# Kernel optimization log

Hardware: AMD Instinct MI355X
Metric: run time of the kernel (lower is better)

The kernel has to match this reference:

```python
import jax, jax.numpy as jnp
import numpy as np

LR, HR, H, D1 = 512, 2048, 4, 200
N = 2 * HR            # 4096 nodes (fully connected graph)
C1 = D1 // H          # 50  per-head dim, layer 1
C2 = HR // H          # 512 per-head dim, layer 2
EPS = 1e-5


def setup_inputs() -> dict:
    key = jax.random.key(0)
    ks = jax.random.split(key, 24)
    lin = lambda k, fi, fo: jax.random.normal(k, (fi, fo), jnp.float32) * 0.02
    vec = lambda k, d: jax.random.normal(k, (d,), jnp.float32) * 0.02
    inp = {"lr_x": jax.random.normal(ks[0], (LR, N), jnp.float32)}
    # TransformerConv 1: lr -> 200 (query/key/value/skip linears, each with bias)
    inp["Wq1"], inp["bq1"] = lin(ks[1], LR, D1), vec(ks[2], D1)
    inp["Wk1"], inp["bk1"] = lin(ks[3], LR, D1), vec(ks[4], D1)
    inp["Wv1"], inp["bv1"] = lin(ks[5], LR, D1), vec(ks[6], D1)
    inp["Ws1"], inp["bs1"] = lin(ks[7], LR, D1), vec(ks[8], D1)
    # GraphNorm 1
    inp["gn1_w"] = 1.0 + 0.1 * jax.random.normal(ks[9], (D1,), jnp.float32)
    inp["gn1_b"] = vec(ks[10], D1)
    inp["gn1_ms"] = 1.0 + 0.1 * jax.random.normal(ks[11], (D1,), jnp.float32)
    # TransformerConv 2: 200 -> 2048
    inp["Wq2"], inp["bq2"] = lin(ks[12], D1, HR), vec(ks[13], HR)
    inp["Wk2"], inp["bk2"] = lin(ks[14], D1, HR), vec(ks[15], HR)
    inp["Wv2"], inp["bv2"] = lin(ks[16], D1, HR), vec(ks[17], HR)
    inp["Ws2"], inp["bs2"] = lin(ks[18], D1, HR), vec(ks[19], HR)
    # GraphNorm 2
    inp["gn2_w"] = 1.0 + 0.1 * jax.random.normal(ks[20], (HR,), jnp.float32)
    inp["gn2_b"] = vec(ks[21], HR)
    inp["gn2_ms"] = 1.0 + 0.1 * jax.random.normal(ks[22], (HR,), jnp.float32)
    return inp


def _transformer_conv(x, Wq, bq, Wk, bk, Wv, bv, Ws, bs, heads, ch):
    # PyG TransformerConv on a fully-connected edge_index == dense multi-head attention
    n = x.shape[0]
    q = (x @ Wq + bq).reshape(n, heads, ch)
    k = (x @ Wk + bk).reshape(n, heads, ch)
    v = (x @ Wv + bv).reshape(n, heads, ch)
    scores = jnp.einsum('ihc,jhc->hij', q, k) / (ch ** 0.5)  # [H, N, N]
    attn = jax.nn.softmax(scores, axis=-1)                   # softmax over source nodes j
    out = jnp.einsum('hij,jhc->ihc', attn, v).reshape(n, heads * ch)
    return out + x @ Ws + bs                                 # root/skip connection


def _graph_norm(x, w, b, ms):
    # PyG GraphNorm: y = w * (x - ms*mean) / sqrt(E[(x - ms*mean)^2] + eps) + b
    mean = jnp.mean(x, axis=0, keepdims=True)
    out = x - mean * ms
    var = jnp.mean(out * out, axis=0, keepdims=True)
    return out * jax.lax.rsqrt(var + EPS) * w + b


def reference(lr_x, Wq1, bq1, Wk1, bk1, Wv1, bv1, Ws1, bs1, gn1_w, gn1_b, gn1_ms,
              Wq2, bq2, Wk2, bk2, Wv2, bv2, Ws2, bs2, gn2_w, gn2_b, gn2_ms):
    h = _transformer_conv(lr_x.T, Wq1, bq1, Wk1, bk1, Wv1, bv1, Ws1, bs1, H, C1)  # [N, 200]
    h = _graph_norm(h, gn1_w, gn1_b, gn1_ms)
    h2 = _transformer_conv(h, Wq2, bq2, Wk2, bk2, Wv2, bv2, Ws2, bs2, H, C2)      # [N, HR]
    h2 = _graph_norm(h2, gn2_w, gn2_b, gn2_ms).T                                  # [HR, N]
    h2 = h2 / jnp.linalg.norm(h2, axis=1, keepdims=True)
    return jax.nn.relu(h2 @ h2.T)                                                 # [HR, HR]
```

## Files before the change

kernel.cpp:

```cpp
#include <hip/hip_runtime.h>
#include <math.h>

typedef unsigned int u32;
typedef unsigned short ushort_t;
typedef __attribute__((ext_vector_type(8))) short short8;
typedef __attribute__((ext_vector_type(4))) float f32x4;

__device__ __forceinline__ ushort_t f2bf(float x) {
  u32 u = __float_as_uint(x);
  u32 r = (u + 0x7fffu + ((u >> 16) & 1u)) >> 16;
  return (ushort_t)r;
}
__device__ __forceinline__ float bf2f(u32 s) {
  return __uint_as_float(s << 16);
}
__device__ __forceinline__ void ld4bf(const ushort_t* p, float* o) {
  uint2 u = *(const uint2*)p;
  o[0] = bf2f(u.x & 0xffffu); o[1] = bf2f(u.x >> 16);
  o[2] = bf2f(u.y & 0xffffu); o[3] = bf2f(u.y >> 16);
}

__device__ __forceinline__ float block_sum256(float v, float* red) {
  #pragma unroll
  for (int o = 32; o > 0; o >>= 1) v += __shfl_down(v, o, 64);
  __syncthreads();
  if ((threadIdx.x & 63) == 0) red[threadIdx.x >> 6] = v;
  __syncthreads();
  return red[0] + red[1] + red[2] + red[3];
}

__global__ __launch_bounds__(512) void fused_attn1(
    const ushort_t* __restrict__ qk, const ushort_t* __restrict__ v,
    float* __restrict__ oP, float* __restrict__ r1p, float scale)
{
  __shared__ ushort_t Kl[2][4096];
  __shared__ ushort_t Vl[2][4096];
  __shared__ ushort_t Pl[128][80];
  const int t = threadIdx.x;
  const int lane = t & 63;
  const int wv = t >> 6;
  const int h = blockIdx.y;
  const int m0 = blockIdx.x * 128;
  const int z = blockIdx.z;
  const int lr = lane & 15;
  const int hk = lane >> 4;

  short8 aq0, aq1;
  {
    const ushort_t* qrow = qk + (size_t)(m0 + wv * 16 + lr) * 512 + h * 64;
    aq0 = *(const short8*)(qrow + hk * 8);
    aq1 = *(const short8*)(qrow + 32 + hk * 8);
  }

  f32x4 oAcc[4];
  #pragma unroll
  for (int i = 0; i < 4; ++i) oAcc[i] = (f32x4){0.f, 0.f, 0.f, 0.f};
  float racc[4] = {0.f, 0.f, 0.f, 0.f};

  const size_t kbase = (size_t)256 + h * 64;
  const int rS = t >> 3;
  const int cS = t & 7;
  const int lcS = cS ^ (rS & 7);

  {
    const int n0 = z * 16 * 64;
    __builtin_amdgcn_global_load_lds(
        (const __attribute__((address_space(1))) u32*)(qk + (size_t)(n0 + rS) * 512 + kbase + lcS * 8),
        (__attribute__((address_space(3))) u32*)(&Kl[0][t * 8]), 16, 0, 0);
    __builtin_amdgcn_global_load_lds(
        (const __attribute__((address_space(1))) u32*)(v + (size_t)(h * 128 + rS) * 4096 + n0 + lcS * 8),
        (__attribute__((address_space(3))) u32*)(&Vl[0][t * 8]), 16, 0, 0);
  }
  __syncthreads();

  int cur = 0;
  for (int it = 0; it < 16; ++it) {
    if (it + 1 < 16) {
      const int n1 = (z * 16 + it + 1) * 64;
      __builtin_amdgcn_global_load_lds(
          (const __attribute__((address_space(1))) u32*)(qk + (size_t)(n1 + rS) * 512 + kbase + lcS * 8),
          (__attribute__((address_space(3))) u32*)(&Kl[cur ^ 1][t * 8]), 16, 0, 0);
      __builtin_amdgcn_global_load_lds(
          (const __attribute__((address_space(1))) u32*)(v + (size_t)(h * 128 + rS) * 4096 + n1 + lcS * 8),
          (__attribute__((address_space(3))) u32*)(&Vl[cur ^ 1][t * 8]), 16, 0, 0);
    }
    f32x4 sA[4];
    #pragma unroll
    for (int nf = 0; nf < 4; ++nf) {
      const int rl = nf * 16 + lr;
      const char* kb = (const char*)&Kl[cur][0] + rl * 128;
      short8 b0 = *(const short8*)(kb + ((hk ^ (rl & 7)) * 16));
      short8 b1 = *(const short8*)(kb + (((4 + hk) ^ (rl & 7)) * 16));
      f32x4 sa = (f32x4){0.f, 0.f, 0.f, 0.f};
      sa = __builtin_amdgcn_mfma_f32_16x16x32_bf16(aq0, b0, sa, 0, 0, 0);
      sa = __builtin_amdgcn_mfma_f32_16x16x32_bf16(aq1, b1, sa, 0, 0, 0);
      sA[nf] = sa;
    }
    #pragma unroll
    for (int nf = 0; nf < 4; ++nf) {
      #pragma unroll
      for (int r = 0; r < 4; ++r) {
        float e = exp2f(sA[nf][r] * scale);
        racc[r] += e;
        Pl[wv * 16 + hk * 4 + r][nf * 16 + lr] = f2bf(e);
      }
    }
    short8 ap0 = *(const short8*)&Pl[wv * 16 + lr][hk * 8];
    short8 ap1 = *(const short8*)&Pl[wv * 16 + lr][32 + hk * 8];
    #pragma unroll
    for (int ff = 0; ff < 4; ++ff) {
      const int rl = ff * 16 + lr;
      const char* vb = (const char*)&Vl[cur][0] + rl * 128;
      short8 b0 = *(const short8*)(vb + ((hk ^ (rl & 7)) * 16));
      short8 b1 = *(const short8*)(vb + (((4 + hk) ^ (rl & 7)) * 16));
      oAcc[ff] = __builtin_amdgcn_mfma_f32_16x16x32_bf16(ap0, b0, oAcc[ff], 0, 0, 0);
      oAcc[ff] = __builtin_amdgcn_mfma_f32_16x16x32_bf16(ap1, b1, oAcc[ff], 0, 0, 0);
    }
    __syncthreads();
    cur ^= 1;
  }

  #pragma unroll
  for (int r = 0; r < 4; ++r) {
    racc[r] += __shfl_xor(racc[r], 1);
    racc[r] += __shfl_xor(racc[r], 2);
    racc[r] += __shfl_xor(racc[r], 4);
    racc[r] += __shfl_xor(racc[r], 8);
  }
  if (lr == 0) {
    float* rp = r1p + ((size_t)z * 4 + h) * 4096;
    #pragma unroll
    for (int r = 0; r < 4; ++r) rp[m0 + wv * 16 + hk * 4 + r] = racc[r];
  }
  float* ob = oP + (size_t)z * 512 * 4096;
  #pragma unroll
  for (int ff = 0; ff < 4; ++ff) {
    const size_t fbase = (size_t)(h * 128 + ff * 16 + lr) * 4096;
    #pragma unroll
    for (int r = 0; r < 4; ++r) {
      const int q = m0 + wv * 16 + hk * 4 + r;
      ob[fbase + q] = oAcc[ff][r];
    }
  }
}

__global__ __launch_bounds__(512, 2) void fused_attn2(
    const ushort_t* __restrict__ Tm, const ushort_t* __restrict__ X,
    const ushort_t* __restrict__ Xt, ushort_t* __restrict__ Up, float scale)
{
  __shared__ ushort_t Xl[16384];
  __shared__ ushort_t Xtl[2][16384];
  __shared__ ushort_t Pl[256][66];
  const int t = threadIdx.x;
  const int lane = t & 63;
  const int wv = t >> 6;
  const int h = blockIdx.y;
  const int m0 = blockIdx.x * 256;
  const int z = blockIdx.z;
  const int lr = lane & 15;
  const int hk = lane >> 4;

  short8 tq[2][8];
  #pragma unroll
  for (int qb = 0; qb < 2; ++qb) {
    const ushort_t* trow = Tm + ((size_t)h * 4096 + m0 + wv * 32 + qb * 16 + lr) * 256;
    #pragma unroll
    for (int s = 0; s < 8; ++s) tq[qb][s] = *(const short8*)(trow + s * 32 + hk * 8);
  }

  f32x4 uAcc[16][2];
  #pragma unroll
  for (int i = 0; i < 16; ++i) {
    uAcc[i][0] = (f32x4){0.f, 0.f, 0.f, 0.f};
    uAcc[i][1] = (f32x4){0.f, 0.f, 0.f, 0.f};
  }

  auto stageX = [&](int n0) {
    #pragma unroll
    for (int i = 0; i < 4; ++i) {
      const int st = t + i * 512;
      const int row = st >> 5, ph = st & 31;
      const int lc = (ph & 24) | ((ph & 7) ^ (row & 7));
      __builtin_amdgcn_global_load_lds(
          (const __attribute__((address_space(1))) u32*)(X + (size_t)(n0 + row) * 256 + lc * 8),
          (__attribute__((address_space(3))) u32*)(&Xl[st * 8]), 16, 0, 0);
    }
  };
  auto stageXt = [&](int buf, int n0) {
    #pragma unroll
    for (int i = 0; i < 4; ++i) {
      const int st = t + i * 512;
      const int row = st >> 3, ph = st & 7;
      const int lc = ph ^ (row & 7);
      __builtin_amdgcn_global_load_lds(
          (const __attribute__((address_space(1))) u32*)(Xt + (size_t)row * 4096 + n0 + lc * 8),
          (__attribute__((address_space(3))) u32*)(&Xtl[buf][st * 8]), 16, 0, 0);
    }
  };

  const int base = z * 16;
  stageX(base * 64);
  stageXt(0, base * 64);
  __syncthreads();

  int cur = 0;
  for (int it = 0; it < 16; ++it) {
    if (it + 1 < 16) stageXt(cur ^ 1, (base + it + 1) * 64);
    const char* xb = (const char*)&Xl[0];
    #pragma unroll
    for (int nf = 0; nf < 4; ++nf) {
      const int row = nf * 16 + lr;
      const char* rb = xb + row * 512;
      f32x4 sa0 = (f32x4){0.f, 0.f, 0.f, 0.f};
      f32x4 sa1 = (f32x4){0.f, 0.f, 0.f, 0.f};
      #pragma unroll
      for (int s = 0; s < 8; ++s) {
        const int c = s * 4 + hk;
        const int ph = (c & 24) | ((c & 7) ^ (row & 7));
        short8 xf = *(const short8*)(rb + ph * 16);
        sa0 = __builtin_amdgcn_mfma_f32_16x16x32_bf16(xf, tq[0][s], sa0, 0, 0, 0);
        sa1 = __builtin_amdgcn_mfma_f32_16x16x32_bf16(xf, tq[1][s], sa1, 0, 0, 0);
      }
      #pragma unroll
      for (int r = 0; r < 4; ++r) {
        Pl[wv * 32 + lr][nf * 16 + hk * 4 + r]      = f2bf(exp2f(sa0[r] * scale));
        Pl[wv * 32 + 16 + lr][nf * 16 + hk * 4 + r] = f2bf(exp2f(sa1[r] * scale));
      }
    }
    __syncthreads();
    if (it + 1 < 16) stageX((base + it + 1) * 64);
    short8 p00 = *(const short8*)((const char*)&Pl[wv * 32 + lr][0] + hk * 16);
    short8 p01 = *(const short8*)((const char*)&Pl[wv * 32 + lr][0] + (4 + hk) * 16);
    short8 p10 = *(const short8*)((const char*)&Pl[wv * 32 + 16 + lr][0] + hk * 16);
    short8 p11 = *(const short8*)((const char*)&Pl[wv * 32 + 16 + lr][0] + (4 + hk) * 16);
    const char* xtb = (const char*)&Xtl[cur][0];
    #pragma unroll
    for (int ff = 0; ff < 16; ++ff) {
      const int row = ff * 16 + lr;
      const char* rb2 = xtb + row * 128;
      short8 x0 = *(const short8*)(rb2 + ((hk ^ (row & 7)) * 16));
      short8 x1 = *(const short8*)(rb2 + (((4 + hk) ^ (row & 7)) * 16));
      uAcc[ff][0] = __builtin_amdgcn_mfma_f32_16x16x32_bf16(x0, p00, uAcc[ff][0], 0, 0, 0);
      uAcc[ff][0] = __builtin_amdgcn_mfma_f32_16x16x32_bf16(x1, p01, uAcc[ff][0], 0, 0, 0);
      uAcc[ff][1] = __builtin_amdgcn_mfma_f32_16x16x32_bf16(x0, p10, uAcc[ff][1], 0, 0, 0);
      uAcc[ff][1] = __builtin_amdgcn_mfma_f32_16x16x32_bf16(x1, p11, uAcc[ff][1], 0, 0, 0);
    }
    __syncthreads();
    cur ^= 1;
  }

  ushort_t* ub = Up + (size_t)(z * 4 + h) * 256 * 4096;
  #pragma unroll
  for (int ff = 0; ff < 16; ++ff) {
    #pragma unroll
    for (int qb = 0; qb < 2; ++qb) {
      #pragma unroll
      for (int r = 0; r < 4; ++r) {
        const int a = ff * 16 + hk * 4 + r;
        ub[(size_t)a * 4096 + m0 + wv * 32 + qb * 16 + lr] = f2bf(uAcc[ff][qb][r]);
      }
    }
  }
}

__global__ __launch_bounds__(256) void combine_u(
    const ushort_t* __restrict__ Up, ushort_t* __restrict__ Usum,
    float* __restrict__ r2)
{
  __shared__ float tl[64][65];
  const int t = threadIdx.x;
  const int qt = blockIdx.x;
  const int at = blockIdx.y;
  const int h  = blockIdx.z;
  const int c = t & 63;
  const int rb = t >> 6;
  const size_t PLN = (size_t)4 * 256 * 4096;
  #pragma unroll
  for (int i = 0; i < 16; ++i) {
    const int r = rb + i * 4;
    const int a = at * 64 + r;
    const int q = qt * 64 + c;
    const size_t i0 = ((size_t)h * 256 + a) * 4096 + q;
    float val = bf2f(Up[i0]) + bf2f(Up[PLN + i0])
              + bf2f(Up[2 * PLN + i0]) + bf2f(Up[3 * PLN + i0]);
    tl[r][c] = val;
    if (a == 200) r2[(size_t)h * 4096 + q] = val;
  }
  __syncthreads();
  #pragma unroll
  for (int i = 0; i < 16; ++i) {
    const int r = rb + i * 4;
    const int q = qt * 64 + r;
    const int a = at * 64 + c;
    Usum[((size_t)h * 4096 + q) * 256 + a] = f2bf(tl[c][r]);
  }
}

#define RD_A(bb, mm, cc) (*(const short8*)(lsAc + (bb)*32768 + arow + (mm)*2048 + (cc)))
#define RD_B(bb, nn, cc) (*(const short8*)(lsBc + (bb)*32768 + brow + (nn)*2048 + (cc)))

#define MM8(nn, bv) { \
  acc[0][nn] = __builtin_amdgcn_mfma_f32_16x16x32_bf16(a0, bv, acc[0][nn], 0,0,0); \
  acc[1][nn] = __builtin_amdgcn_mfma_f32_16x16x32_bf16(a1, bv, acc[1][nn], 0,0,0); \
  acc[2][nn] = __builtin_amdgcn_mfma_f32_16x16x32_bf16(a2, bv, acc[2][nn], 0,0,0); \
  acc[3][nn] = __builtin_amdgcn_mfma_f32_16x16x32_bf16(a3, bv, acc[3][nn], 0,0,0); \
  acc[4][nn] = __builtin_amdgcn_mfma_f32_16x16x32_bf16(a4, bv, acc[4][nn], 0,0,0); \
  acc[5][nn] = __builtin_amdgcn_mfma_f32_16x16x32_bf16(a5, bv, acc[5][nn], 0,0,0); \
  acc[6][nn] = __builtin_amdgcn_mfma_f32_16x16x32_bf16(a6, bv, acc[6][nn], 0,0,0); \
  acc[7][nn] = __builtin_amdgcn_mfma_f32_16x16x32_bf16(a7, bv, acc[7][nn], 0,0,0); }

#define STG(BASE, LD, LS, bb, hf, tt) { \
  _Pragma("unroll") \
  for (int ii = 0; ii < 2; ++ii) { \
    const int s_ = t + ii * 512; \
    const int r_ = s_ >> 3; \
    const int lc_ = (s_ & 7) ^ (r_ & 7); \
    __builtin_amdgcn_global_load_lds( \
      (const __attribute__((address_space(1))) u32*)((BASE) + (size_t)((hf) * 128 + r_) * (LD) + (size_t)(tt) * 64 + lc_ * 8), \
      (__attribute__((address_space(3))) u32*)(&(LS)[bb][(hf) * 8192 + s_ * 8]), 16, 0, 0); \
  } }

#define BAR() __builtin_amdgcn_s_barrier()
#define PRIO(x) __builtin_amdgcn_s_setprio(x)

#define GRP(bf, tS1, tS2) { \
  a0=RD_A(bf,0,c0); a1=RD_A(bf,1,c0); a2=RD_A(bf,2,c0); a3=RD_A(bf,3,c0); \
  a4=RD_A(bf,4,c0); a5=RD_A(bf,5,c0); a6=RD_A(bf,6,c0); a7=RD_A(bf,7,c0); \
  b0=RD_B(bf,0,c0); b1=RD_B(bf,1,c0); \
  STG(Ab, lda, lsA, 1-(bf), 1, tS1); STG(Bb, ldb, lsB, 1-(bf), 0, tS1); \
  BAR(); PRIO(1); MM8(0, b0); MM8(1, b1); PRIO(0); BAR(); \
  b2=RD_B(bf,2,c0); b3=RD_B(bf,3,c0); \
  STG(Bb, ldb, lsB, 1-(bf), 1, tS1); \
  BAR(); PRIO(1); MM8(2, b2); MM8(3, b3); PRIO(0); BAR(); \
  a0=RD_A(bf,0,c1); a1=RD_A(bf,1,c1); a2=RD_A(bf,2,c1); a3=RD_A(bf,3,c1); \
  a4=RD_A(bf,4,c1); a5=RD_A(bf,5,c1); a6=RD_A(bf,6,c1); a7=RD_A(bf,7,c1); \
  b0=RD_B(bf,0,c1); b1=RD_B(bf,1,c1); \
  BAR(); PRIO(1); MM8(0, b0); MM8(1, b1); PRIO(0); BAR(); \
  b2=RD_B(bf,2,c1); b3=RD_B(bf,3,c1); \
  STG(Ab, lda, lsA, (bf), 0, tS2); \
  BAR(); PRIO(1); MM8(2, b2); MM8(3, b3); PRIO(0); \
  asm volatile("s_waitcnt vmcnt(2)" ::: "memory"); \
  BAR(); }

template<int CMODE, bool RELU>
__global__ __launch_bounds__(512, 2) void mfma256_8ph(
    const ushort_t* __restrict__ A, const ushort_t* __restrict__ B,
    void* __restrict__ Cv, int lda, int ldb, int ldc,
    int K, int zsplit, size_t zA, size_t zB, size_t zC,
    int bShift, size_t bHead, int Mvalid, float scale)
{
  __shared__ ushort_t lsA[2][16384];
  __shared__ ushort_t lsB[2][16384];
  const int t = threadIdx.x;
  const int gx = gridDim.x;
  const int nwg = gx * gridDim.y;
  const int bid = blockIdx.y * gx + blockIdx.x;
  const int qq = nwg >> 3, rr_ = nwg & 7;
  const int xcd = bid & 7, idx = bid >> 3;
  const int swz = (xcd < rr_ ? xcd * (qq + 1) : rr_ * (qq + 1) + (xcd - rr_) * qq) + idx;
  const int m0 = (swz / gx) * 256;
  const int n0 = (swz % gx) * 256;
  const int z = blockIdx.z;
  int Kc = K, kOff = 0;
  size_t aZ = 0, bZ = 0, cZ = 0;
  if (zsplit > 1) { Kc = K / zsplit; kOff = z * Kc; cZ = (size_t)z * zC; }
  else { aZ = (size_t)z * zA; bZ = (size_t)z * zB; cZ = (size_t)z * zC; }
  const ushort_t* Ab = A + aZ + (size_t)m0 * lda + kOff;
  const ushort_t* Bb = B + bZ + (size_t)n0 * ldb + kOff
                     + (bShift >= 0 ? (size_t)(m0 >> bShift) * bHead : 0);
  const int NT = Kc / 64;

  f32x4 acc[8][4];
  #pragma unroll
  for (int i = 0; i < 8; ++i)
    #pragma unroll
    for (int j = 0; j < 4; ++j) acc[i][j] = (f32x4){0.f, 0.f, 0.f, 0.f};

  const int lane = t & 63;
  const int wv = t >> 6;
  const int wr = (wv >> 2) * 128;
  const int wc = (wv & 3) * 64;
  const int lr = lane & 15;
  const int kc = lane >> 4;
  const int sw = lane & 7;
  const int c0 = (kc ^ sw) * 16;
  const int c1 = c0 ^ 64;
  const int arow = (wr + lr) * 128;
  const int brow = (wc + lr) * 128;
  const char* lsAc = (const char*)lsA;
  const char* lsBc = (const char*)lsB;

  short8 a0, a1, a2, a3, a4, a5, a6, a7, b0, b1, b2, b3;

  STG(Ab, lda, lsA, 0, 0, 0); STG(Ab, lda, lsA, 0, 1, 0);
  STG(Bb, ldb, lsB, 0, 0, 0); STG(Bb, ldb, lsB, 0, 1, 0);
  STG(Ab, lda, lsA, 1, 0, 1);
  asm volatile("s_waitcnt vmcnt(2)" ::: "memory");
  BAR();

  const int NITER = NT >> 1;
  for (int it = 0; it < NITER; ++it) {
    const int tb = 2 * it;
    const int s1 = tb + 1;
    const int s2 = (tb + 2 < NT) ? tb + 2 : 0;
    const int s3 = (tb + 3 < NT) ? tb + 3 : 0;
    GRP(0, s1, s2)
    GRP(1, s2, s3)
  }

  const int row4 = (lane >> 4) * 4;
  const int coln = lane & 15;
  float* Cf = (float*)Cv + cZ;
  ushort_t* Ch = (ushort_t*)Cv + cZ;
  #pragma unroll
  for (int m = 0; m < 8; ++m) {
    #pragma unroll
    for (int r = 0; r < 4; ++r) {
      const int gm = m0 + wr + m * 16 + row4 + r;
      const bool ok = gm < Mvalid;
      #pragma unroll
      for (int n = 0; n < 4; ++n) {
        const int gn = n0 + wc + n * 16 + coln;
        float v = acc[m][n][r] * scale;
        if (RELU) v = fmaxf(v, 0.f);
        if (ok) {
          if (CMODE == 0)      Cf[(size_t)gm * ldc + gn] = v;
          else if (CMODE == 1) Ch[(size_t)gm * ldc + gn] = f2bf(v);
          else                 atomicAdd(&Cf[(size_t)gm * ldc + gn], v);
        }
      }
    }
  }
}

#undef GRP
#undef STG
#undef MM8
#undef RD_A
#undef RD_B

template<int CMODE, bool RELU>
__global__ __launch_bounds__(256) void mfma_bt(
    const ushort_t* __restrict__ A, const ushort_t* __restrict__ B,
    void* __restrict__ Cv, int lda, int ldb, int ldc,
    int K, int Ksplit, size_t zA, size_t zB, size_t zC,
    int bShift, size_t bHead, int mMask, int Mvalid, float scale)
{
  __shared__ ushort_t lsA[2][128 * 32];
  __shared__ ushort_t lsB[2][128 * 32];
  const int t  = threadIdx.x;
  const int m0 = blockIdx.y * 128;
  const int n0 = blockIdx.x * 128;
  const int z = blockIdx.z;
  int Kc = K, kOff = 0;
  size_t aZ = 0, bZ = 0, cZ = 0;
  if (Ksplit > 1) { Kc = K / Ksplit; kOff = z * Kc; cZ = (size_t)z * zC; }
  else { aZ = (size_t)z * zA; bZ = (size_t)z * zB; cZ = (size_t)z * zC; }
  const int NT = Kc / 32;
  const ushort_t* Ab = A + aZ + (size_t)m0 * lda + kOff;
  const ushort_t* Bb = B + bZ + (size_t)n0 * ldb + kOff
                     + (bShift >= 0 ? (size_t)(m0 >> bShift) * bHead : 0);
  const int cs = t & 3;

  f32x4 acc[4][4];
  #pragma unroll
  for (int i = 0; i < 4; ++i)
    #pragma unroll
    for (int j = 0; j < 4; ++j) acc[i][j] = (f32x4){0.f, 0.f, 0.f, 0.f};

  const int lane = t & 63;
  const int wv = t >> 6;
  const int wr = (wv >> 1) * 64;
  const int wc = (wv & 1) * 64;
  const int lr = lane & 15;
  const int kc = lane >> 4;

  int roffA[4], roffB[4];
  #pragma unroll
  for (int m = 0; m < 4; ++m) {
    int ra = wr + m * 16 + lr;
    roffA[m] = ra * 64 + ((kc ^ (ra & 3)) * 16);
    int rb = wc + m * 16 + lr;
    roffB[m] = rb * 64 + ((kc ^ (rb & 3)) * 16);
  }

  auto stage = [&](int buf, int kt) {
    const ushort_t* As = Ab + kt * 32;
    const ushort_t* Bs = Bb + kt * 32;
    #pragma unroll
    for (int i = 0; i < 2; ++i) {
      int s = t + i * 256;
      int r = s >> 2;
      int c = cs ^ (r & 3);
      __builtin_amdgcn_global_load_lds(
          (const __attribute__((address_space(1))) u32*)(As + (size_t)r * lda + c * 8),
          (__attribute__((address_space(3))) u32*)(&lsA[buf][s * 8]), 16, 0, 0);
    }
    #pragma unroll
    for (int i = 0; i < 2; ++i) {
      int s = t + i * 256;
      int r = s >> 2;
      int c = cs ^ (r & 3);
      __builtin_amdgcn_global_load_lds(
          (const __attribute__((address_space(1))) u32*)(Bs + (size_t)r * ldb + c * 8),
          (__attribute__((address_space(3))) u32*)(&lsB[buf][s * 8]), 16, 0, 0);
    }
  };

  stage(0, 0);
  __syncthreads();
  int cur = 0;
  for (int kt = 0; kt < NT; ++kt) {
    if (kt + 1 < NT) stage(cur ^ 1, kt + 1);
    short8 af[4], bfr[4];
    const char* baseA = (const char*)&lsA[cur][0];
    const char* baseB = (const char*)&lsB[cur][0];
    #pragma unroll
    for (int m = 0; m < 4; ++m) af[m]  = *(const short8*)(baseA + roffA[m]);
    #pragma unroll
    for (int n = 0; n < 4; ++n) bfr[n] = *(const short8*)(baseB + roffB[n]);
    #pragma unroll
    for (int m = 0; m < 4; ++m)
      #pragma unroll
      for (int n = 0; n < 4; ++n)
        acc[m][n] = __builtin_amdgcn_mfma_f32_16x16x32_bf16(af[m], bfr[n], acc[m][n], 0, 0, 0);
    __syncthreads();
    cur ^= 1;
  }

  const int row4 = (lane >> 4) * 4;
  const int coln = lane & 15;
  float* Cf = (float*)Cv + cZ;
  ushort_t* Ch = (ushort_t*)Cv + cZ;
  #pragma unroll
  for (int m = 0; m < 4; ++m) {
    #pragma unroll
    for (int r = 0; r < 4; ++r) {
      const int gm = m0 + wr + m * 16 + row4 + r;
      const bool ok = (mMask >= 0) ? ((gm & mMask) < Mvalid) : (gm < Mvalid);
      #pragma unroll
      for (int n = 0; n < 4; ++n) {
        const int gn = n0 + wc + n * 16 + coln;
        float v = acc[m][n][r] * scale;
        if (RELU) v = fmaxf(v, 0.f);
        if (ok) {
          if (CMODE == 0)      Cf[(size_t)gm * ldc + gn] = v;
          else if (CMODE == 1) Ch[(size_t)gm * ldc + gn] = f2bf(v);
          else                 atomicAdd(&Cf[(size_t)gm * ldc + gn], v);
        }
      }
    }
  }
}

__global__ __launch_bounds__(256) void wt_conv(
    const float* __restrict__ W, const float* __restrict__ bias,
    ushort_t* __restrict__ dst, int Mtot, int ldw, int Kv, int Kp,
    int PADH, int VALH)
{
  const int m = blockIdx.x;
  const int h = m / PADH, c0 = m % PADH;
  const int fout = h * VALH + c0;
  const bool valid = (c0 < VALH) && (fout < Mtot);
  for (int k = threadIdx.x; k < Kp; k += blockDim.x) {
    float v = 0.f;
    if (valid) {
      if (k < Kv) v = W[(size_t)k * ldw + fout];
      else if (k == Kv) v = bias[fout];
    }
    dst[(size_t)m * Kp + k] = f2bf(v);
  }
}

__global__ __launch_bounds__(256) void wt_trans(
    const float* __restrict__ W, const float* __restrict__ bias,
    ushort_t* __restrict__ dst)
{
  const int rid = blockIdx.x;
  const int h = rid >> 8, a = rid & 255;
  for (int f = threadIdx.x; f < 512; f += 256) {
    float v = 0.f;
    if (a < 200)       v = W[(size_t)a * 2048 + h * 512 + f];
    else if (a == 200) v = bias[h * 512 + f];
    dst[(size_t)rid * 512 + f] = f2bf(v);
  }
}

__global__ __launch_bounds__(256) void xt_conv(
    const float* __restrict__ h1nT, ushort_t* __restrict__ Xt)
{
  const int a = blockIdx.x;
  for (int q = threadIdx.x; q < 4096; q += 256) {
    float v = (a < 200) ? h1nT[(size_t)a * 4096 + q] : ((a == 200) ? 1.f : 0.f);
    Xt[(size_t)a * 4096 + q] = f2bf(v);
  }
}

__global__ __launch_bounds__(256) void trans_pad(
    const float* __restrict__ src, ushort_t* __restrict__ dst, int Kv, int Kp)
{
  __shared__ float tl[64][65];
  const int t = threadIdx.x;
  const int f0 = blockIdx.x * 64;
  const int i0 = blockIdx.y * 64;
  const int c = t & 63, rbase = t >> 6;
  #pragma unroll
  for (int it = 0; it < 16; ++it) {
    int r = rbase + it * 4;
    int f = f0 + r;
    tl[r][c] = (f < Kv) ? src[(size_t)f * 4096 + i0 + c] : 0.f;
  }
  __syncthreads();
  #pragma unroll
  for (int it = 0; it < 16; ++it) {
    int r = rbase + it * 4;
    int f = f0 + c;
    if (f < Kp) {
      float v = (f < Kv) ? tl[c][r] : ((f == Kv) ? 1.f : 0.f);
      dst[(size_t)(i0 + r) * Kp + f] = f2bf(v);
    }
  }
}

__global__ __launch_bounds__(256) void graph_norm_attn1(
    const float* __restrict__ skip, const float* __restrict__ oP,
    const float* __restrict__ r1p, float* __restrict__ out,
    const float* __restrict__ w, const float* __restrict__ b,
    const float* __restrict__ ms)
{
  __shared__ float red[4];
  const int t = threadIdx.x;
  const int row = blockIdx.x;
  const int h = row / 50;
  const int pr = h * 128 + row % 50;
  const float* sk = skip + (size_t)pr * 4096;
  const size_t OSTR = (size_t)512 * 4096;
  float v[16];
  float s = 0.f;
  #pragma unroll
  for (int e = 0; e < 4; ++e) {
    const int idx = t * 4 + 1024 * e;
    float4 a = *(const float4*)&sk[idx];
    float4 o0 = *(const float4*)&oP[(size_t)pr * 4096 + idx];
    float4 o1 = *(const float4*)&oP[OSTR + (size_t)pr * 4096 + idx];
    float4 o2 = *(const float4*)&oP[2 * OSTR + (size_t)pr * 4096 + idx];
    float4 o3 = *(const float4*)&oP[3 * OSTR + (size_t)pr * 4096 + idx];
    float4 r0 = *(const float4*)&r1p[(size_t)h * 4096 + idx];
    float4 r1 = *(const float4*)&r1p[(size_t)(4 + h) * 4096 + idx];
    float4 r2 = *(const float4*)&r1p[(size_t)(8 + h) * 4096 + idx];
    float4 r3 = *(const float4*)&r1p[(size_t)(12 + h) * 4096 + idx];
    v[e*4+0] = a.x + (o0.x + o1.x + o2.x + o3.x) / (r0.x + r1.x + r2.x + r3.x);
    v[e*4+1] = a.y + (o0.y + o1.y + o2.y + o3.y) / (r0.y + r1.y + r2.y + r3.y);
    v[e*4+2] = a.z + (o0.z + o1.z + o2.z + o3.z) / (r0.z + r1.z + r2.z + r3.z);
    v[e*4+3] = a.w + (o0.w + o1.w + o2.w + o3.w) / (r0.w + r1.w + r2.w + r3.w);
    s += v[e*4+0] + v[e*4+1] + v[e*4+2] + v[e*4+3];
  }
  const float mean = block_sum256(s, red) * (1.f / 4096.f);
  const float sub = mean * ms[row];
  float s2 = 0.f;
  #pragma unroll
  for (int e = 0; e < 16; ++e) { v[e] -= sub; s2 += v[e] * v[e]; }
  const float var = block_sum256(s2, red) * (1.f / 4096.f);
  const float scl = rsqrtf(var + 1e-5f) * w[row];
  const float bb = b[row];
  float* y = out + (size_t)row * 4096;
  #pragma unroll
  for (int e = 0; e < 4; ++e) {
    float o0[4];
    #pragma unroll
    for (int q = 0; q < 4; ++q) o0[q] = v[e * 4 + q] * scl + bb;
    *(float4*)&y[t * 4 + 1024 * e] = *(float4*)&o0[0];
  }
}

__global__ __launch_bounds__(256) void graph_norm_attn2(
    const ushort_t* __restrict__ skip, const ushort_t* __restrict__ O,
    const float* __restrict__ r2, ushort_t* __restrict__ out,
    const float* __restrict__ w, const float* __restrict__ b,
    const float* __restrict__ ms)
{
  __shared__ float red[4];
  const int t = threadIdx.x;
  const int row = blockIdx.x;
  const ushort_t* sk = skip + (size_t)row * 4096;
  const ushort_t* pa = O + (size_t)row * 4096;
  const float* rr = r2 + (size_t)(row >> 9) * 4096;
  float v[16];
  float s = 0.f;
  #pragma unroll
  for (int e = 0; e < 4; ++e) {
    const int idx = t * 4 + 1024 * e;
    float a[4], oa[4];
    ld4bf(&sk[idx], a); ld4bf(&pa[idx], oa);
    float4 rv = *(const float4*)&rr[idx];
    v[e*4+0] = a[0] + oa[0] / rv.x;
    v[e*4+1] = a[1] + oa[1] / rv.y;
    v[e*4+2] = a[2] + oa[2] / rv.z;
    v[e*4+3] = a[3] + oa[3] / rv.w;
    s += v[e*4+0] + v[e*4+1] + v[e*4+2] + v[e*4+3];
  }
  const float mean = block_sum256(s, red) * (1.f / 4096.f);
  const float sub = mean * ms[row];
  float s2 = 0.f;
  #pragma unroll
  for (int e = 0; e < 16; ++e) { v[e] -= sub; s2 += v[e] * v[e]; }
  const float var = block_sum256(s2, red) * (1.f / 4096.f);
  const float scl = rsqrtf(var + 1e-5f) * w[row];
  const float bb = b[row];
  #pragma unroll
  for (int e = 0; e < 16; ++e) v[e] = v[e] * scl + bb;
  float s3 = 0.f;
  #pragma unroll
  for (int e = 0; e < 16; ++e) s3 += v[e] * v[e];
  const float osc = rsqrtf(block_sum256(s3, red));
  ushort_t* y = out + (size_t)row * 4096;
  #pragma unroll
  for (int e = 0; e < 4; ++e) {
    ushort_t o0[4];
    #pragma unroll
    for (int q = 0; q < 4; ++q) o0[q] = f2bf(v[e * 4 + q] * osc);
    *(ushort2*)&y[t * 4 + 1024 * e] = *(ushort2*)&o0[0];
    *(ushort2*)&y[t * 4 + 1024 * e + 2] = *(ushort2*)&o0[2];
  }
}

__global__ __launch_bounds__(256) void add4_relu_bf16(
    const ushort_t* __restrict__ g, float* __restrict__ out)
{
  const size_t i = (size_t)blockIdx.x * 256 + threadIdx.x;
  const size_t ss = (size_t)2048 * 2048;
  float a[4], b[4], c[4], d[4];
  ld4bf(&g[i * 4], a);
  ld4bf(&g[ss + i * 4], b);
  ld4bf(&g[2 * ss + i * 4], c);
  ld4bf(&g[3 * ss + i * 4], d);
  float4 o;
  o.x = fmaxf(a[0] + b[0] + c[0] + d[0], 0.f);
  o.y = fmaxf(a[1] + b[1] + c[1] + d[1], 0.f);
  o.z = fmaxf(a[2] + b[2] + c[2] + d[2], 0.f);
  o.w = fmaxf(a[3] + b[3] + c[3] + d[3], 0.f);
  ((float4*)out)[i] = o;
}

extern "C" void kernel_launch(void* const* d_in, const int* in_sizes, int n_in,
                              void* d_out, int out_size, void* d_ws, size_t ws_size,
                              hipStream_t stream)
{
  (void)in_sizes; (void)n_in; (void)out_size; (void)ws_size;
  const float* lr_x = (const float*)d_in[0];
  const float* Wq1 = (const float*)d_in[1];  const float* bq1 = (const float*)d_in[2];
  const float* Wk1 = (const float*)d_in[3];  const float* bk1 = (const float*)d_in[4];
  const float* Wv1 = (const float*)d_in[5];  const float* bv1 = (const float*)d_in[6];
  const float* Ws1 = (const float*)d_in[7];  const float* bs1 = (const float*)d_in[8];
  const float* gn1w = (const float*)d_in[9]; const float* gn1b = (const float*)d_in[10];
  const float* gn1ms = (const float*)d_in[11];
  const float* Wq2 = (const float*)d_in[12]; const float* bq2 = (const float*)d_in[13];
  const float* Wk2 = (const float*)d_in[14]; const float* bk2 = (const float*)d_in[15];
  const float* Wv2 = (const float*)d_in[16]; const float* bv2 = (const float*)d_in[17];
  const float* Ws2 = (const float*)d_in[18]; const float* bs2 = (const float*)d_in[19];
  const float* gn2w = (const float*)d_in[20]; const float* gn2b = (const float*)d_in[21];
  const float* gn2ms = (const float*)d_in[22];

  char* p = (char*)d_ws;
  auto alloc = [&](size_t bytes) { char* r = p; p += (bytes + 255) & ~(size_t)255; return r; };
  char*     scrA = alloc((size_t)32 * 1024 * 1024);
  ushort_t* xb   = (ushort_t*)alloc((size_t)4096 * 544 * 2);
  ushort_t* qk1b = (ushort_t*)alloc((size_t)4096 * 512 * 2);
  ushort_t* v1b  = (ushort_t*)alloc((size_t)512 * 4096 * 2);
  char*     u0   = alloc((size_t)16 * 1024 * 1024);
  float*    s1p  = (float*)u0;
  float*    h1nT = (float*)   alloc((size_t)200 * 4096 * 4);
  ushort_t* h1nb = (ushort_t*)alloc((size_t)4096 * 256 * 2);
  ushort_t* Wqk1 = (ushort_t*)alloc((size_t)512 * 544 * 2);
  ushort_t* Wv1b = (ushort_t*)alloc((size_t)512 * 544 * 2);
  ushort_t* Ws1p = (ushort_t*)alloc((size_t)512 * 544 * 2);
  ushort_t* Wcat = (ushort_t*)alloc((size_t)4096 * 256 * 2);
  ushort_t* Qt   = (ushort_t*)alloc((size_t)4 * 256 * 512 * 2);
  ushort_t* Kt   = (ushort_t*)alloc((size_t)4 * 256 * 512 * 2);
  ushort_t* Mtall= (ushort_t*)alloc((size_t)4 * 256 * 256 * 2);
  ushort_t* Tall = (ushort_t*)alloc((size_t)4 * 4096 * 256 * 2);
  ushort_t* Xtb  = (ushort_t*)alloc((size_t)256 * 4096 * 2);
  ushort_t* vs2b = (ushort_t*)alloc((size_t)4096 * 4096 * 2);
  ushort_t* Usum = (ushort_t*)alloc((size_t)4 * 4096 * 256 * 2);
  ushort_t* Opl  = (ushort_t*)alloc((size_t)2048 * 4096 * 2);
  float*    r1p  = (float*)   alloc((size_t)16 * 4096 * 4);
  float*    r2   = (float*)   alloc((size_t)4 * 4096 * 4);
  float*    oP   = (float*)scrA;
  ushort_t* UpH  = (ushort_t*)scrA;
  ushort_t* g4   = (ushort_t*)scrA;
  ushort_t* h2b  = (ushort_t*)u0;

  const dim3 b256(256, 1, 1);
  const dim3 b512(512, 1, 1);
  const float LOG2E = 1.4426950408889634f;
  const float sc1e = 0.14142135623730951f * LOG2E;
  const float sc2e = 0.04419417382415922f * LOG2E;

  wt_conv<<<dim3(256),  b256, 0, stream>>>(Wq1, bq1, Wqk1,             200, 200, 512, 544, 64, 50);
  wt_conv<<<dim3(256),  b256, 0, stream>>>(Wk1, bk1, Wqk1 + 256 * 544, 200, 200, 512, 544, 64, 50);
  wt_conv<<<dim3(512),  b256, 0, stream>>>(Wv1, bv1, Wv1b,             200, 200, 512, 544, 128, 50);
  wt_conv<<<dim3(512),  b256, 0, stream>>>(Ws1, bs1, Ws1p,             200, 200, 512, 544, 128, 50);
  wt_conv<<<dim3(2048), b256, 0, stream>>>(Wv2, bv2, Wcat,              2048, 2048, 200, 256, 2048, 2048);
  wt_conv<<<dim3(2048), b256, 0, stream>>>(Ws2, bs2, Wcat + 2048 * 256, 2048, 2048, 200, 256, 2048, 2048);
  wt_trans<<<dim3(1024), b256, 0, stream>>>(Wq2, bq2, Qt);
  wt_trans<<<dim3(1024), b256, 0, stream>>>(Wk2, bk2, Kt);
  trans_pad<<<dim3(9, 64), b256, 0, stream>>>(lr_x, xb, 512, 544);

  mfma_bt<1, false><<<dim3(4, 32), b256, 0, stream>>>(
      xb, Wqk1, qk1b, 544, 544, 512, 544, 1, 0, 0, 0, -1, 0, -1, 4096, 1.f);
  mfma_bt<1, false><<<dim3(32, 4), b256, 0, stream>>>(
      Wv1b, xb, v1b, 544, 544, 4096, 544, 1, 0, 0, 0, -1, 0, -1, 512, 1.f);
  mfma_bt<0, false><<<dim3(32, 4), b256, 0, stream>>>(
      Ws1p, xb, s1p, 544, 544, 4096, 544, 1, 0, 0, 0, -1, 0, 127, 50, 1.f);

  fused_attn1<<<dim3(32, 4, 4), b512, 0, stream>>>(qk1b, v1b, oP, r1p, sc1e);
  graph_norm_attn1<<<dim3(200), b256, 0, stream>>>(s1p, oP, r1p, h1nT, gn1w, gn1b, gn1ms);
  trans_pad<<<dim3(4, 64), b256, 0, stream>>>(h1nT, h1nb, 200, 256);
  xt_conv<<<dim3(256), b256, 0, stream>>>(h1nT, Xtb);

  mfma_bt<1, false><<<dim3(32, 32), b256, 0, stream>>>(
      Wcat, h1nb, vs2b, 256, 256, 4096, 256, 1, 0, 0, 0, -1, 0, -1, 4096, 1.f);

  mfma_bt<1, false><<<dim3(2, 2, 4), b256, 0, stream>>>(
      Kt, Qt, Mtall, 512, 512, 256, 512, 1,
      (size_t)256 * 512, (size_t)256 * 512, (size_t)256 * 256, -1, 0, -1, 256, 1.f);
  mfma_bt<1, false><<<dim3(2, 32, 4), b256, 0, stream>>>(
      h1nb, Mtall, Tall, 256, 256, 256, 256, 1,
      0, (size_t)256 * 256, (size_t)4096 * 256, -1, 0, -1, 4096, 1.f);
  fused_attn2<<<dim3(16, 4, 4), b512, 0, stream>>>(Tall, h1nb, Xtb, UpH, sc2e);
  combine_u<<<dim3(64, 4, 4), b256, 0, stream>>>(UpH, Usum, r2);
  mfma_bt<1, false><<<dim3(32, 16), b256, 0, stream>>>(
      Wcat, Usum, Opl, 256, 256, 4096, 256, 1,
      0, 0, 0, 9, (size_t)4096 * 256, -1, 2048, 1.f);
  graph_norm_attn2<<<dim3(2048), b256, 0, stream>>>(
      vs2b + (size_t)2048 * 4096, Opl, r2, h2b, gn2w, gn2b, gn2ms);

  mfma256_8ph<1, false><<<dim3(8, 8, 4), b512, 0, stream>>>(
      h2b, h2b, g4, 4096, 4096, 2048, 4096, 4,
      0, 0, (size_t)2048 * 2048, -1, 0, 2048, 1.f);
  add4_relu_bf16<<<dim3(4096), b256, 0, stream>>>(g4, (float*)d_out);
}
```

Before: 350.5 us.

## Trim padded layer-2 K dimension to 224 and merge V1/skip GEMMs

Layer 2's inner dimension is 200, padded to 256. The fused attention kernel and several GEMMs now loop over only 224 of those columns (7 k-steps and 14 feature tiles instead of 8 and 16), which skips MFMA work and accumulators on zero padding. The layer-1 value and skip projections are merged into one GEMM writing bf16, and graph_norm_attn1 now reads the skip term as bf16 instead of fp32. The risks are that any data living in columns 224–255 (such as the bias column at index 200) must fall inside the kept range, that the Up rows for features 224–255 are no longer written, and that the skip term loses precision.

```diff
diff --git a/kernel.cpp b/kernel.cpp
--- a/kernel.cpp
+++ b/kernel.cpp
@@ -160,17 +160,17 @@
   const int lr = lane & 15;
   const int hk = lane >> 4;
 
-  short8 tq[2][8];
+  short8 tq[2][7];
   #pragma unroll
   for (int qb = 0; qb < 2; ++qb) {
     const ushort_t* trow = Tm + ((size_t)h * 4096 + m0 + wv * 32 + qb * 16 + lr) * 256;
     #pragma unroll
-    for (int s = 0; s < 8; ++s) tq[qb][s] = *(const short8*)(trow + s * 32 + hk * 8);
-  }
-
-  f32x4 uAcc[16][2];
-  #pragma unroll
-  for (int i = 0; i < 16; ++i) {
+    for (int s = 0; s < 7; ++s) tq[qb][s] = *(const short8*)(trow + s * 32 + hk * 8);
+  }
+
+  f32x4 uAcc[14][2];
+  #pragma unroll
+  for (int i = 0; i < 14; ++i) {
     uAcc[i][0] = (f32x4){0.f, 0.f, 0.f, 0.f};
     uAcc[i][1] = (f32x4){0.f, 0.f, 0.f, 0.f};
   }
@@ -214,7 +214,7 @@
       f32x4 sa0 = (f32x4){0.f, 0.f, 0.f, 0.f};
       f32x4 sa1 = (f32x4){0.f, 0.f, 0.f, 0.f};
       #pragma unroll
-      for (int s = 0; s < 8; ++s) {
+      for (int s = 0; s < 7; ++s) {
         const int c = s * 4 + hk;
         const int ph = (c & 24) | ((c & 7) ^ (row & 7));
         short8 xf = *(const short8*)(rb + ph * 16);
@@ -235,7 +235,7 @@
     short8 p11 = *(const short8*)((const char*)&Pl[wv * 32 + 16 + lr][0] + (4 + hk) * 16);
     const char* xtb = (const char*)&Xtl[cur][0];
     #pragma unroll
-    for (int ff = 0; ff < 16; ++ff) {
+    for (int ff = 0; ff < 14; ++ff) {
       const int row = ff * 16 + lr;
       const char* rb2 = xtb + row * 128;
       short8 x0 = *(const short8*)(rb2 + ((hk ^ (row & 7)) * 16));
@@ -251,7 +251,7 @@
 
   ushort_t* ub = Up + (size_t)(z * 4 + h) * 256 * 4096;
   #pragma unroll
-  for (int ff = 0; ff < 16; ++ff) {
+  for (int ff = 0; ff < 14; ++ff) {
     #pragma unroll
     for (int qb = 0; qb < 2; ++qb) {
       #pragma unroll
@@ -623,7 +623,7 @@
 }
 
 __global__ __launch_bounds__(256) void graph_norm_attn1(
-    const float* __restrict__ skip, const float* __restrict__ oP,
+    const ushort_t* __restrict__ skip, const float* __restrict__ oP,
     const float* __restrict__ r1p, float* __restrict__ out,
     const float* __restrict__ w, const float* __restrict__ b,
     const float* __restrict__ ms)
@@ -633,14 +633,15 @@
   const int row = blockIdx.x;
   const int h = row / 50;
   const int pr = h * 128 + row % 50;
-  const float* sk = skip + (size_t)pr * 4096;
+  const ushort_t* sk = skip + (size_t)pr * 4096;
   const size_t OSTR = (size_t)512 * 4096;
   float v[16];
   float s = 0.f;
   #pragma unroll
   for (int e = 0; e < 4; ++e) {
     const int idx = t * 4 + 1024 * e;
-    float4 a = *(const float4*)&sk[idx];
+    float a[4];
+    ld4bf(&sk[idx], a);
     float4 o0 = *(const float4*)&oP[(size_t)pr * 4096 + idx];
     float4 o1 = *(const float4*)&oP[OSTR + (size_t)pr * 4096 + idx];
     float4 o2 = *(const float4*)&oP[2 * OSTR + (size_t)pr * 4096 + idx];
@@ -649,10 +650,10 @@
     float4 r1 = *(const float4*)&r1p[(size_t)(4 + h) * 4096 + idx];
     float4 r2 = *(const float4*)&r1p[(size_t)(8 + h) * 4096 + idx];
     float4 r3 = *(const float4*)&r1p[(size_t)(12 + h) * 4096 + idx];
-    v[e*4+0] = a.x + (o0.x + o1.x + o2.x + o3.x) / (r0.x + r1.x + r2.x + r3.x);
-    v[e*4+1] = a.y + (o0.y + o1.y + o2.y + o3.y) / (r0.y + r1.y + r2.y + r3.y);
-    v[e*4+2] = a.z + (o0.z + o1.z + o2.z + o3.z) / (r0.z + r1.z + r2.z + r3.z);
-    v[e*4+3] = a.w + (o0.w + o1.w + o2.w + o3.w) / (r0.w + r1.w + r2.w + r3.w);
+    v[e*4+0] = a[0] + (o0.x + o1.x + o2.x + o3.x) / (r0.x + r1.x + r2.x + r3.x);
+    v[e*4+1] = a[1] + (o0.y + o1.y + o2.y + o3.y) / (r0.y + r1.y + r2.y + r3.y);
+    v[e*4+2] = a[2] + (o0.z + o1.z + o2.z + o3.z) / (r0.z + r1.z + r2.z + r3.z);
+    v[e*4+3] = a[3] + (o0.w + o1.w + o2.w + o3.w) / (r0.w + r1.w + r2.w + r3.w);
     s += v[e*4+0] + v[e*4+1] + v[e*4+2] + v[e*4+3];
   }
   const float mean = block_sum256(s, red) * (1.f / 4096.f);
@@ -766,14 +767,12 @@
   char*     scrA = alloc((size_t)32 * 1024 * 1024);
   ushort_t* xb   = (ushort_t*)alloc((size_t)4096 * 544 * 2);
   ushort_t* qk1b = (ushort_t*)alloc((size_t)4096 * 512 * 2);
-  ushort_t* v1b  = (ushort_t*)alloc((size_t)512 * 4096 * 2);
+  ushort_t* v1s  = (ushort_t*)alloc((size_t)1024 * 4096 * 2);
   char*     u0   = alloc((size_t)16 * 1024 * 1024);
-  float*    s1p  = (float*)u0;
   float*    h1nT = (float*)   alloc((size_t)200 * 4096 * 4);
   ushort_t* h1nb = (ushort_t*)alloc((size_t)4096 * 256 * 2);
   ushort_t* Wqk1 = (ushort_t*)alloc((size_t)512 * 544 * 2);
-  ushort_t* Wv1b = (ushort_t*)alloc((size_t)512 * 544 * 2);
-  ushort_t* Ws1p = (ushort_t*)alloc((size_t)512 * 544 * 2);
+  ushort_t* Wvs1 = (ushort_t*)alloc((size_t)1024 * 544 * 2);
   ushort_t* Wcat = (ushort_t*)alloc((size_t)4096 * 256 * 2);
   ushort_t* Qt   = (ushort_t*)alloc((size_t)4 * 256 * 512 * 2);
   ushort_t* Kt   = (ushort_t*)alloc((size_t)4 * 256 * 512 * 2);
@@ -798,8 +797,8 @@
 
   wt_conv<<<dim3(256),  b256, 0, stream>>>(Wq1, bq1, Wqk1,             200, 200, 512, 544, 64, 50);
   wt_conv<<<dim3(256),  b256, 0, stream>>>(Wk1, bk1, Wqk1 + 256 * 544, 200, 200, 512, 544, 64, 50);
-  wt_conv<<<dim3(512),  b256, 0, stream>>>(Wv1, bv1, Wv1b,             200, 200, 512, 544, 128, 50);
-  wt_conv<<<dim3(512),  b256, 0, stream>>>(Ws1, bs1, Ws1p,             200, 200, 512, 544, 128, 50);
+  wt_conv<<<dim3(512),  b256, 0, stream>>>(Wv1, bv1, Wvs1,             200, 200, 512, 544, 128, 50);
+  wt_conv<<<dim3(512),  b256, 0, stream>>>(Ws1, bs1, Wvs1 + 512 * 544, 200, 200, 512, 544, 128, 50);
   wt_conv<<<dim3(2048), b256, 0, stream>>>(Wv2, bv2, Wcat,              2048, 2048, 200, 256, 2048, 2048);
   wt_conv<<<dim3(2048), b256, 0, stream>>>(Ws2, bs2, Wcat + 2048 * 256, 2048, 2048, 200, 256, 2048, 2048);
   wt_trans<<<dim3(1024), b256, 0, stream>>>(Wq2, bq2, Qt);
@@ -808,29 +807,28 @@
 
   mfma_bt<1, false><<<dim3(4, 32), b256, 0, stream>>>(
       xb, Wqk1, qk1b, 544, 544, 512, 544, 1, 0, 0, 0, -1, 0, -1, 4096, 1.f);
-  mfma_bt<1, false><<<dim3(32, 4), b256, 0, stream>>>(
-      Wv1b, xb, v1b, 544, 544, 4096, 544, 1, 0, 0, 0, -1, 0, -1, 512, 1.f);
-  mfma_bt<0, false><<<dim3(32, 4), b256, 0, stream>>>(
-      Ws1p, xb, s1p, 544, 544, 4096, 544, 1, 0, 0, 0, -1, 0, 127, 50, 1.f);
-
-  fused_attn1<<<dim3(32, 4, 4), b512, 0, stream>>>(qk1b, v1b, oP, r1p, sc1e);
-  graph_norm_attn1<<<dim3(200), b256, 0, stream>>>(s1p, oP, r1p, h1nT, gn1w, gn1b, gn1ms);
+  mfma_bt<1, false><<<dim3(32, 8), b256, 0, stream>>>(
+      Wvs1, xb, v1s, 544, 544, 4096, 544, 1, 0, 0, 0, -1, 0, -1, 1024, 1.f);
+
+  fused_attn1<<<dim3(32, 4, 4), b512, 0, stream>>>(qk1b, v1s, oP, r1p, sc1e);
+  graph_norm_attn1<<<dim3(200), b256, 0, stream>>>(
+      v1s + (size_t)512 * 4096, oP, r1p, h1nT, gn1w, gn1b, gn1ms);
   trans_pad<<<dim3(4, 64), b256, 0, stream>>>(h1nT, h1nb, 200, 256);
   xt_conv<<<dim3(256), b256, 0, stream>>>(h1nT, Xtb);
 
   mfma_bt<1, false><<<dim3(32, 32), b256, 0, stream>>>(
-      Wcat, h1nb, vs2b, 256, 256, 4096, 256, 1, 0, 0, 0, -1, 0, -1, 4096, 1.f);
+      Wcat, h1nb, vs2b, 256, 256, 4096, 224, 1, 0, 0, 0, -1, 0, -1, 4096, 1.f);
 
   mfma_bt<1, false><<<dim3(2, 2, 4), b256, 0, stream>>>(
       Kt, Qt, Mtall, 512, 512, 256, 512, 1,
       (size_t)256 * 512, (size_t)256 * 512, (size_t)256 * 256, -1, 0, -1, 256, 1.f);
   mfma_bt<1, false><<<dim3(2, 32, 4), b256, 0, stream>>>(
-      h1nb, Mtall, Tall, 256, 256, 256, 256, 1,
+      h1nb, Mtall, Tall, 256, 256, 256, 224, 1,
       0, (size_t)256 * 256, (size_t)4096 * 256, -1, 0, -1, 4096, 1.f);
   fused_attn2<<<dim3(16, 4, 4), b512, 0, stream>>>(Tall, h1nb, Xtb, UpH, sc2e);
   combine_u<<<dim3(64, 4, 4), b256, 0, stream>>>(UpH, Usum, r2);
   mfma_bt<1, false><<<dim3(32, 16), b256, 0, stream>>>(
-      Wcat, Usum, Opl, 256, 256, 4096, 256, 1,
+      Wcat, Usum, Opl, 256, 256, 4096, 224, 1,
       0, 0, 0, 9, (size_t)4096 * 256, -1, 2048, 1.f);
   graph_norm_attn2<<<dim3(2048), b256, 0, stream>>>(
       vs2b + (size_t)2048 * 4096, Opl, r2, h2b, gn2w, gn2b, gn2ms);
```

After: 328.1 us. -6.4%, faster.
